# Kernel tuning notes

Hardware: AMD Instinct MI355X
Metric: run time of the kernel (lower is better)

## Reference

```python
import jax, jax.numpy as jnp
import numpy as np
import math

B, S, D, H = 1, 4096, 512, 8


def setup_inputs() -> dict:
    key = jax.random.key(0)
    ks = jax.random.split(key, 7)
    s = 0.02
    return {
        "queries": jax.random.normal(ks[0], (B, S, D), jnp.float32),
        "keys": jax.random.normal(ks[1], (B, S, D), jnp.float32),
        "values": jax.random.normal(ks[2], (B, S, D), jnp.float32),
        "Wq": jax.random.normal(ks[3], (D, D), jnp.float32) * s,
        "Wk": jax.random.normal(ks[4], (D, D), jnp.float32) * s,
        "Wv": jax.random.normal(ks[5], (D, D), jnp.float32) * s,
        "Wo": jax.random.normal(ks[6], (D, D), jnp.float32) * s,
    }


def _split_heads(x, num_heads):
    # (B, S, D) -> (B*H, S, D/H), matching transpose_qkv
    b, s, d = x.shape
    x = x.reshape(b, s, num_heads, d // num_heads).transpose(0, 2, 1, 3)
    return x.reshape(b * num_heads, s, d // num_heads)


def _merge_heads(x, num_heads):
    # (B*H, S, dh) -> (B, S, D), matching transpose_output
    bh, s, dh = x.shape
    x = x.reshape(bh // num_heads, num_heads, s, dh).transpose(0, 2, 1, 3)
    return x.reshape(bh // num_heads, s, num_heads * dh)


def reference(queries, keys, values, Wq, Wk, Wv, Wo):
    q = _split_heads(queries @ Wq.T, H)  # (B*H, S, dh)
    k = _split_heads(keys @ Wk.T, H)
    v = _split_heads(values @ Wv.T, H)
    dh = q.shape[-1]
    scores = jnp.einsum('bqd,bkd->bqk', q, k) / math.sqrt(dh)  # (B*H, Sq, Sk)
    # NOTE: original torch code applies softmax over dim=0 (the batch*heads axis).
    attn = jax.nn.softmax(scores, axis=0)
    out = jnp.einsum('bqk,bkd->bqd', attn, v)  # dropout p=0 -> identity
    out = _merge_heads(out, H)  # (B, S, D)
    return out @ Wo.T
```

## Files before the change

kernel.cpp:

```cpp
#include <hip/hip_runtime.h>

constexpr int S_ = 4096;
constexpr int D_ = 512;
constexpr int NJC = 4;
constexpr int JC = S_ / NJC;

using f32x4 = __attribute__((ext_vector_type(4))) float;
using s16x8 = __attribute__((ext_vector_type(8))) short;
using u16x4 = __attribute__((ext_vector_type(4))) unsigned short;
using u16x8 = __attribute__((ext_vector_type(8))) unsigned short;

__device__ __forceinline__ unsigned short f2bf(float f) {
    union { float f; unsigned u; } v; v.f = f;
    unsigned r = v.u + 0x7FFFu + ((v.u >> 16) & 1u);
    return (unsigned short)(r >> 16);
}

template<bool IN_BF16, int OUT_MODE>
__global__ __launch_bounds__(256) void proj_kernel(const void* __restrict__ Xv,
                                                   const float* __restrict__ W,
                                                   void* __restrict__ Yv) {
    constexpr int BM = 128, BN = 64, BK = 64;
    __shared__ unsigned short Xs[BM][BK + 8];
    __shared__ unsigned short Ws_[BN][BK + 8];
    const int m0 = blockIdx.x * BM;
    const int n0 = blockIdx.y * BN;
    const int tid = threadIdx.x;
    const int lane = tid & 63, w = tid >> 6;
    const int wi = w >> 1, wj = w & 1;
    const int lr = lane & 15, lg = lane >> 4;

    f32x4 acc[4][2] = {};

    for (int kt = 0; kt < D_ / BK; ++kt) {
        const int k0 = kt * BK;
        __syncthreads();
        if (IN_BF16) {
            const unsigned short* X = (const unsigned short*)Xv;
#pragma unroll
            for (int r = 0; r < 4; ++r) {
                int idx = tid + r * 256;
                int row = idx >> 3, c8 = idx & 7;
                u16x8 vv = *(const u16x8*)(X + (size_t)(m0 + row) * D_ + k0 + c8 * 8);
                *(u16x8*)&Xs[row][c8 * 8] = vv;
            }
        } else {
            const float* X = (const float*)Xv;
#pragma unroll
            for (int r = 0; r < 8; ++r) {
                int idx = tid + r * 256;
                int row = idx >> 4, c4 = idx & 15;
                f32x4 vv = *(const f32x4*)(X + (size_t)(m0 + row) * D_ + k0 + c4 * 4);
                u16x4 o;
#pragma unroll
                for (int t = 0; t < 4; ++t) o[t] = f2bf(vv[t]);
                *(u16x4*)&Xs[row][c4 * 4] = o;
            }
        }
#pragma unroll
        for (int r = 0; r < 4; ++r) {
            int idx = tid + r * 256;
            int row = idx >> 4, c4 = idx & 15;
            f32x4 vv = *(const f32x4*)(W + (size_t)(n0 + row) * D_ + k0 + c4 * 4);
            u16x4 o;
#pragma unroll
            for (int t = 0; t < 4; ++t) o[t] = f2bf(vv[t]);
            *(u16x4*)&Ws_[row][c4 * 4] = o;
        }
        __syncthreads();
#pragma unroll
        for (int ks = 0; ks < 2; ++ks) {
            s16x8 a[4], b[2];
#pragma unroll
            for (int mf = 0; mf < 4; ++mf)
                a[mf] = *(const s16x8*)&Xs[wi * 64 + mf * 16 + lr][ks * 32 + lg * 8];
#pragma unroll
            for (int nf = 0; nf < 2; ++nf)
                b[nf] = *(const s16x8*)&Ws_[wj * 32 + nf * 16 + lr][ks * 32 + lg * 8];
#pragma unroll
            for (int mf = 0; mf < 4; ++mf)
#pragma unroll
                for (int nf = 0; nf < 2; ++nf)
                    acc[mf][nf] = __builtin_amdgcn_mfma_f32_16x16x32_bf16(a[mf], b[nf], acc[mf][nf], 0, 0, 0);
        }
    }

    if (OUT_MODE == 1) {
        __syncthreads();
        unsigned short* T = &Xs[0][0] + w * 2304;
#pragma unroll
        for (int mf = 0; mf < 4; ++mf)
#pragma unroll
            for (int nf = 0; nf < 2; ++nf)
#pragma unroll
                for (int r = 0; r < 4; ++r) {
                    int n_loc = nf * 16 + lr;
                    int i_loc = mf * 16 + lg * 4 + r;
                    T[n_loc * 72 + i_loc] = f2bf(acc[mf][nf][r]);
                }
        __syncthreads();
        unsigned short* Y = (unsigned short*)Yv;
#pragma unroll
        for (int rr = 0; rr < 4; ++rr) {
            int chunk = lane + rr * 64;
            int n_loc = chunk >> 3, c8 = chunk & 7;
            u16x8 vv = *(const u16x8*)&T[n_loc * 72 + c8 * 8];
            *(u16x8*)(Y + (size_t)(n0 + wj * 32 + n_loc) * S_ + m0 + wi * 64 + c8 * 8) = vv;
        }
    } else {
#pragma unroll
        for (int mf = 0; mf < 4; ++mf)
#pragma unroll
            for (int nf = 0; nf < 2; ++nf)
#pragma unroll
                for (int r = 0; r < 4; ++r) {
                    int i = m0 + wi * 64 + mf * 16 + lg * 4 + r;
                    int n = n0 + wj * 32 + nf * 16 + lr;
                    float val = acc[mf][nf][r];
                    if (OUT_MODE == 0) ((unsigned short*)Yv)[(size_t)i * D_ + n] = f2bf(val);
                    else                ((float*)Yv)[(size_t)i * D_ + n] = val;
                }
    }
}

__global__ __launch_bounds__(256) void attn_kernel(const unsigned short* __restrict__ Qp,
                                                   const unsigned short* __restrict__ Kp,
                                                   const unsigned short* __restrict__ VpT,
                                                   float* __restrict__ partial) {
    constexpr int BI = 32, BJ = 32;
    __shared__ unsigned short Qs[BI][520];
    __shared__ unsigned short Es[8][BI][40];
    const int i0 = blockIdx.x * BI;
    const int jc = blockIdx.y;
    const int tid = threadIdx.x;
    const int lane = tid & 63, w = tid >> 6;
    const int lr = lane & 15, lg = lane >> 4;
    const int qi = (w >> 1) * 16, qj = (w & 1) * 16;

#pragma unroll
    for (int r = 0; r < 8; ++r) {
        int idx = tid + r * 256;
        int row = idx >> 6, c8 = idx & 63;
        u16x8 vv = *(const u16x8*)(Qp + (size_t)(i0 + row) * D_ + c8 * 8);
        *(u16x8*)&Qs[row][c8 * 8] = vv;
    }

    f32x4 out[2][2][4] = {};

    for (int t = 0; t < JC / BJ; ++t) {
        const int j0 = jc * JC + t * BJ;
        __syncthreads();

        f32x4 sfrag[8];
#pragma unroll
        for (int h = 0; h < 8; ++h) {
            f32x4 sf = {0.f, 0.f, 0.f, 0.f};
#pragma unroll
            for (int ks = 0; ks < 2; ++ks) {
                s16x8 a = *(const s16x8*)&Qs[qi + lr][h * 64 + ks * 32 + lg * 8];
                s16x8 b = *(const s16x8*)(Kp + (size_t)(j0 + qj + lr) * D_ + h * 64 + ks * 32 + lg * 8);
                sf = __builtin_amdgcn_mfma_f32_16x16x32_bf16(a, b, sf, 0, 0, 0);
            }
            sfrag[h] = sf;
        }
#pragma unroll
        for (int r = 0; r < 4; ++r) {
            float e[8], den = 0.f;
#pragma unroll
            for (int h = 0; h < 8; ++h) { e[h] = __expf(sfrag[h][r] * 0.125f); den += e[h]; }
            float rd = __builtin_amdgcn_rcpf(den);
            int i_loc = qi + lg * 4 + r, j_loc = qj + lr;
#pragma unroll
            for (int h = 0; h < 8; ++h)
                Es[h][i_loc][j_loc] = f2bf(e[h] * rd);
        }
        __syncthreads();

#pragma unroll
        for (int hh = 0; hh < 2; ++hh) {
            int h = 2 * w + hh;
            s16x8 b[4];
#pragma unroll
            for (int df = 0; df < 4; ++df)
                b[df] = *(const s16x8*)(VpT + (size_t)(h * 64 + df * 16 + lr) * S_ + j0 + lg * 8);
#pragma unroll
            for (int mf = 0; mf < 2; ++mf) {
                s16x8 a = *(const s16x8*)&Es[h][mf * 16 + lr][lg * 8];
#pragma unroll
                for (int df = 0; df < 4; ++df)
                    out[hh][mf][df] = __builtin_amdgcn_mfma_f32_16x16x32_bf16(a, b[df], out[hh][mf][df], 0, 0, 0);
            }
        }
    }

    float* P = partial + (size_t)jc * S_ * D_;
#pragma unroll
    for (int hh = 0; hh < 2; ++hh) {
        int h = 2 * w + hh;
#pragma unroll
        for (int mf = 0; mf < 2; ++mf)
#pragma unroll
            for (int df = 0; df < 4; ++df)
#pragma unroll
                for (int r = 0; r < 4; ++r) {
                    int i = i0 + mf * 16 + lg * 4 + r;
                    int d = h * 64 + df * 16 + lr;
                    P[(size_t)i * D_ + d] = out[hh][mf][df][r];
                }
    }
}

__global__ __launch_bounds__(256) void reduce4_kernel(const float* __restrict__ partial,
                                                      unsigned short* __restrict__ outp) {
    size_t base = ((size_t)blockIdx.x * 256 + threadIdx.x) * 4;
    f32x4 s = *(const f32x4*)(partial + base);
#pragma unroll
    for (int c = 1; c < NJC; ++c) {
        f32x4 vv = *(const f32x4*)(partial + (size_t)c * S_ * D_ + base);
        s += vv;
    }
    u16x4 o;
#pragma unroll
    for (int t = 0; t < 4; ++t) o[t] = f2bf(s[t]);
    *(u16x4*)(outp + base) = o;
}

extern "C" void kernel_launch(void* const* d_in, const int* in_sizes, int n_in,
                              void* d_out, int out_size, void* d_ws, size_t ws_size,
                              hipStream_t stream) {
    const float* q  = (const float*)d_in[0];
    const float* k  = (const float*)d_in[1];
    const float* v  = (const float*)d_in[2];
    const float* Wq = (const float*)d_in[3];
    const float* Wk = (const float*)d_in[4];
    const float* Wv = (const float*)d_in[5];
    const float* Wo = (const float*)d_in[6];

    char* ws = (char*)d_ws;
    unsigned short* Qp  = (unsigned short*)(ws);
    unsigned short* Kp  = (unsigned short*)(ws + (4u  << 20));
    unsigned short* VpT = (unsigned short*)(ws + (8u  << 20));
    float*          part= (float*)        (ws + (12u << 20));
    unsigned short* ao  = (unsigned short*)(ws + (44u << 20));

    dim3 pb(256);
    dim3 pg(S_ / 128, D_ / 64);
    proj_kernel<false, 0><<<pg, pb, 0, stream>>>(q, Wq, Qp);
    proj_kernel<false, 0><<<pg, pb, 0, stream>>>(k, Wk, Kp);
    proj_kernel<false, 1><<<pg, pb, 0, stream>>>(v, Wv, VpT);
    attn_kernel<<<dim3(S_ / 32, NJC), pb, 0, stream>>>(Qp, Kp, VpT, part);
    reduce4_kernel<<<dim3(S_ * D_ / 1024), pb, 0, stream>>>(part, ao);
    proj_kernel<true, 2><<<pg, pb, 0, stream>>>(ao, Wo, (float*)d_out);
}
```

Before: 257.0 us.

## Restructure attention kernel to 16-row query tiles with 128-thread blocks and swizzled LDS

The attention kernel now uses 16-query tiles and 2-wave blocks, giving more blocks in flight. The score MFMA operands are swapped so K comes from global memory and Q from an XOR-swizzled LDS buffer, which avoids bank conflicts. Probabilities are packed two bf16 per store into a smaller shared buffer. The split count along the key axis is now a runtime value (2, 4 or 6) picked from workspace size, and the reduce kernel loops over it. This trades more partial-sum traffic and more K/V re-reads per query row for higher occupancy.

```diff
diff --git a/kernel.cpp b/kernel.cpp
--- a/kernel.cpp
+++ b/kernel.cpp
@@ -1,9 +1,8 @@
 #include <hip/hip_runtime.h>
+#include <hip/hip_bf16.h>
 
 constexpr int S_ = 4096;
 constexpr int D_ = 512;
-constexpr int NJC = 4;
-constexpr int JC = S_ / NJC;
 
 using f32x4 = __attribute__((ext_vector_type(4))) float;
 using s16x8 = __attribute__((ext_vector_type(8))) short;
@@ -14,6 +13,12 @@
     union { float f; unsigned u; } v; v.f = f;
     unsigned r = v.u + 0x7FFFu + ((v.u >> 16) & 1u);
     return (unsigned short)(r >> 16);
+}
+
+__device__ __forceinline__ unsigned pack_bf16(float lo, float hi) {
+    float2 t; t.x = lo; t.y = hi;
+    __hip_bfloat162 b = __float22bfloat162_rn(t);
+    union { __hip_bfloat162 b; unsigned u; } cv; cv.b = b; return cv.u;
 }
 
 template<bool IN_BF16, int OUT_MODE>
@@ -123,99 +128,98 @@
     }
 }
 
-__global__ __launch_bounds__(256) void attn_kernel(const unsigned short* __restrict__ Qp,
-                                                   const unsigned short* __restrict__ Kp,
-                                                   const unsigned short* __restrict__ VpT,
-                                                   float* __restrict__ partial) {
-    constexpr int BI = 32, BJ = 32;
-    __shared__ unsigned short Qs[BI][520];
-    __shared__ unsigned short Es[8][BI][40];
-    const int i0 = blockIdx.x * BI;
+__global__ __launch_bounds__(128, 3) void attn_kernel(const unsigned short* __restrict__ Qp,
+                                                      const unsigned short* __restrict__ Kp,
+                                                      const unsigned short* __restrict__ VpT,
+                                                      float* __restrict__ partial, int njc) {
+    __shared__ unsigned char Qlds[16 * 1024];
+    __shared__ unsigned short Es[8][16][40];
+    const int i0 = blockIdx.x * 16;
     const int jc = blockIdx.y;
     const int tid = threadIdx.x;
     const int lane = tid & 63, w = tid >> 6;
     const int lr = lane & 15, lg = lane >> 4;
-    const int qi = (w >> 1) * 16, qj = (w & 1) * 16;
 
 #pragma unroll
     for (int r = 0; r < 8; ++r) {
-        int idx = tid + r * 256;
-        int row = idx >> 6, c8 = idx & 63;
-        u16x8 vv = *(const u16x8*)(Qp + (size_t)(i0 + row) * D_ + c8 * 8);
-        *(u16x8*)&Qs[row][c8 * 8] = vv;
-    }
-
-    f32x4 out[2][2][4] = {};
-
-    for (int t = 0; t < JC / BJ; ++t) {
-        const int j0 = jc * JC + t * BJ;
-        __syncthreads();
-
-        f32x4 sfrag[8];
+        int idx = tid + r * 128;
+        int row = idx >> 6, c16 = idx & 63;
+        u16x8 vv = *(const u16x8*)(Qp + (size_t)(i0 + row) * D_ + c16 * 8);
+        *(u16x8*)&Qlds[row * 1024 + ((c16 * 16) ^ ((row & 7) << 4))] = vv;
+    }
+    __syncthreads();
+
+    f32x4 acc[4][4] = {};
+    const int t0 = (jc * 128) / njc;
+    const int t1 = ((jc + 1) * 128) / njc;
+
+    for (int t = t0; t < t1; ++t) {
+        const int jq = t * 32 + w * 16;
+        f32x4 sf[8];
 #pragma unroll
         for (int h = 0; h < 8; ++h) {
-            f32x4 sf = {0.f, 0.f, 0.f, 0.f};
+            f32x4 s = {0.f, 0.f, 0.f, 0.f};
 #pragma unroll
             for (int ks = 0; ks < 2; ++ks) {
-                s16x8 a = *(const s16x8*)&Qs[qi + lr][h * 64 + ks * 32 + lg * 8];
-                s16x8 b = *(const s16x8*)(Kp + (size_t)(j0 + qj + lr) * D_ + h * 64 + ks * 32 + lg * 8);
-                sf = __builtin_amdgcn_mfma_f32_16x16x32_bf16(a, b, sf, 0, 0, 0);
-            }
-            sfrag[h] = sf;
-        }
+                s16x8 a = *(const s16x8*)(Kp + (size_t)(jq + lr) * D_ + h * 64 + ks * 32 + lg * 8);
+                s16x8 b = *(const s16x8*)&Qlds[lr * 1024 +
+                              (((h * 128 + ks * 64 + lg * 16)) ^ ((lr & 7) << 4))];
+                s = __builtin_amdgcn_mfma_f32_16x16x32_bf16(a, b, s, 0, 0, 0);
+            }
+            sf[h] = s;
+        }
+        float p[8][4];
 #pragma unroll
         for (int r = 0; r < 4; ++r) {
             float e[8], den = 0.f;
 #pragma unroll
-            for (int h = 0; h < 8; ++h) { e[h] = __expf(sfrag[h][r] * 0.125f); den += e[h]; }
+            for (int h = 0; h < 8; ++h) { e[h] = __expf(sf[h][r] * 0.125f); den += e[h]; }
             float rd = __builtin_amdgcn_rcpf(den);
-            int i_loc = qi + lg * 4 + r, j_loc = qj + lr;
-#pragma unroll
-            for (int h = 0; h < 8; ++h)
-                Es[h][i_loc][j_loc] = f2bf(e[h] * rd);
-        }
-        __syncthreads();
-
-#pragma unroll
-        for (int hh = 0; hh < 2; ++hh) {
-            int h = 2 * w + hh;
-            s16x8 b[4];
-#pragma unroll
-            for (int df = 0; df < 4; ++df)
-                b[df] = *(const s16x8*)(VpT + (size_t)(h * 64 + df * 16 + lr) * S_ + j0 + lg * 8);
-#pragma unroll
-            for (int mf = 0; mf < 2; ++mf) {
-                s16x8 a = *(const s16x8*)&Es[h][mf * 16 + lr][lg * 8];
-#pragma unroll
-                for (int df = 0; df < 4; ++df)
-                    out[hh][mf][df] = __builtin_amdgcn_mfma_f32_16x16x32_bf16(a, b[df], out[hh][mf][df], 0, 0, 0);
+#pragma unroll
+            for (int h = 0; h < 8; ++h) p[h][r] = e[h] * rd;
+        }
+        __syncthreads();
+#pragma unroll
+        for (int h = 0; h < 8; ++h) {
+            uint2 d;
+            d.x = pack_bf16(p[h][0], p[h][1]);
+            d.y = pack_bf16(p[h][2], p[h][3]);
+            *(uint2*)&Es[h][lr][w * 16 + lg * 4] = d;
+        }
+        __syncthreads();
+        const int jt = t * 32;
+#pragma unroll
+        for (int hh = 0; hh < 4; ++hh) {
+            int h = w * 4 + hh;
+            s16x8 pa = *(const s16x8*)&Es[h][lr][lg * 8];
+#pragma unroll
+            for (int df = 0; df < 4; ++df) {
+                s16x8 b = *(const s16x8*)(VpT + (size_t)(h * 64 + df * 16 + lr) * S_ + jt + lg * 8);
+                acc[hh][df] = __builtin_amdgcn_mfma_f32_16x16x32_bf16(pa, b, acc[hh][df], 0, 0, 0);
             }
         }
     }
 
     float* P = partial + (size_t)jc * S_ * D_;
 #pragma unroll
-    for (int hh = 0; hh < 2; ++hh) {
-        int h = 2 * w + hh;
-#pragma unroll
-        for (int mf = 0; mf < 2; ++mf)
-#pragma unroll
-            for (int df = 0; df < 4; ++df)
-#pragma unroll
-                for (int r = 0; r < 4; ++r) {
-                    int i = i0 + mf * 16 + lg * 4 + r;
-                    int d = h * 64 + df * 16 + lr;
-                    P[(size_t)i * D_ + d] = out[hh][mf][df][r];
-                }
-    }
-}
-
-__global__ __launch_bounds__(256) void reduce4_kernel(const float* __restrict__ partial,
-                                                      unsigned short* __restrict__ outp) {
+    for (int hh = 0; hh < 4; ++hh) {
+        int h = w * 4 + hh;
+#pragma unroll
+        for (int df = 0; df < 4; ++df)
+#pragma unroll
+            for (int r = 0; r < 4; ++r) {
+                int i = i0 + lg * 4 + r;
+                int d = h * 64 + df * 16 + lr;
+                P[(size_t)i * D_ + d] = acc[hh][df][r];
+            }
+    }
+}
+
+__global__ __launch_bounds__(256) void reduceN_kernel(const float* __restrict__ partial,
+                                                      unsigned short* __restrict__ outp, int njc) {
     size_t base = ((size_t)blockIdx.x * 256 + threadIdx.x) * 4;
     f32x4 s = *(const f32x4*)(partial + base);
-#pragma unroll
-    for (int c = 1; c < NJC; ++c) {
+    for (int c = 1; c < njc; ++c) {
         f32x4 vv = *(const f32x4*)(partial + (size_t)c * S_ * D_ + base);
         s += vv;
     }
@@ -236,19 +240,23 @@
     const float* Wv = (const float*)d_in[5];
     const float* Wo = (const float*)d_in[6];
 
+    int njc = 2;
+    if      (ws_size >= ((size_t)(16 + 8 * 6) << 20)) njc = 6;
+    else if (ws_size >= ((size_t)(16 + 8 * 4) << 20)) njc = 4;
+
     char* ws = (char*)d_ws;
     unsigned short* Qp  = (unsigned short*)(ws);
     unsigned short* Kp  = (unsigned short*)(ws + (4u  << 20));
     unsigned short* VpT = (unsigned short*)(ws + (8u  << 20));
     float*          part= (float*)        (ws + (12u << 20));
-    unsigned short* ao  = (unsigned short*)(ws + (44u << 20));
+    unsigned short* ao  = (unsigned short*)(ws + ((size_t)(12 + 8 * njc) << 20));
 
     dim3 pb(256);
     dim3 pg(S_ / 128, D_ / 64);
     proj_kernel<false, 0><<<pg, pb, 0, stream>>>(q, Wq, Qp);
     proj_kernel<false, 0><<<pg, pb, 0, stream>>>(k, Wk, Kp);
     proj_kernel<false, 1><<<pg, pb, 0, stream>>>(v, Wv, VpT);
-    attn_kernel<<<dim3(S_ / 32, NJC), pb, 0, stream>>>(Qp, Kp, VpT, part);
-    reduce4_kernel<<<dim3(S_ * D_ / 1024), pb, 0, stream>>>(part, ao);
+    attn_kernel<<<dim3(S_ / 16, njc), dim3(128), 0, stream>>>(Qp, Kp, VpT, part, njc);
+    reduceN_kernel<<<dim3(S_ * D_ / 1024), pb, 0, stream>>>(part, ao, njc);
     proj_kernel<true, 2><<<pg, pb, 0, stream>>>(ao, Wo, (float*)d_out);
 }
```

Result: slower. 306.3 us (+19.2%).
